# Performance work log

Hardware: AMD Instinct MI355X
Metric: run time of the kernel (lower is better)

Reference implementation:

```python
import jax, jax.numpy as jnp
from jax import lax
import numpy as np

N, F_IN, D_MODEL = 8192, 128, 256
D_INNER, D_STATE, D_CONV, DT_RANK = 512, 16, 4, 16  # expand=2, d_state=16, d_conv=4, dt_rank=ceil(256/16)
BN_EPS = 1e-5


def setup_inputs() -> dict:
    key = jax.random.key(0)
    ks = jax.random.split(key, 12)
    rn = lambda k, s, sc: jax.random.normal(k, s, jnp.float32) * sc
    x = rn(ks[0], (N, F_IN), 1.0)
    # normalized dense adjacency (row sums ~1)
    adj = jax.random.uniform(ks[1], (N, N), jnp.float32) * (2.0 / N)
    w_gcn = rn(ks[2], (F_IN, D_MODEL), 1.0 / np.sqrt(F_IN))
    b_gcn = rn(ks[3], (D_MODEL,), 0.02)
    bn_gamma = jnp.ones((D_MODEL,), jnp.float32)
    bn_beta = jnp.zeros((D_MODEL,), jnp.float32)
    w_in = rn(ks[4], (2 * D_INNER, D_MODEL), 1.0 / np.sqrt(D_MODEL))
    conv_w = rn(ks[5], (D_INNER, D_CONV), 1.0 / np.sqrt(D_CONV))
    conv_b = rn(ks[6], (D_INNER,), 0.02)
    w_xproj = rn(ks[7], (DT_RANK + 2 * D_STATE, D_INNER), 1.0 / np.sqrt(D_INNER))
    w_dt = rn(ks[8], (D_INNER, DT_RANK), 1.0 / np.sqrt(DT_RANK))
    b_dt = rn(ks[9], (D_INNER,), 0.1)
    A_log = jnp.log(jnp.broadcast_to(jnp.arange(1, D_STATE + 1, dtype=jnp.float32), (D_INNER, D_STATE)))
    D_skip = jnp.ones((D_INNER,), jnp.float32)
    w_out = rn(ks[10], (D_MODEL, D_INNER), 1.0 / np.sqrt(D_INNER))
    return dict(x=x, adj=adj, w_gcn=w_gcn, b_gcn=b_gcn, bn_gamma=bn_gamma, bn_beta=bn_beta,
                w_in=w_in, conv_w=conv_w, conv_b=conv_b, w_xproj=w_xproj, w_dt=w_dt,
                b_dt=b_dt, A_log=A_log, D_skip=D_skip, w_out=w_out)


def _forward(x, adj, w_gcn, b_gcn, bn_gamma, bn_beta, w_in, conv_w, conv_b,
             w_xproj, w_dt, b_dt, A_log, D_skip, w_out):
    # --- GCN layer: adj @ (x @ W) + b ---
    h = adj @ (x @ w_gcn) + b_gcn            # (N, D_MODEL)
    h = jax.nn.relu(h)
    # dropout: eval mode -> identity
    # --- BatchNorm1d (batch statistics, biased var, as torch training norm) ---
    mean = jnp.mean(h, axis=0)
    var = jnp.var(h, axis=0)
    h = (h - mean) * lax.rsqrt(var + BN_EPS) * bn_gamma + bn_beta  # (N, D_MODEL)

    # --- Mamba block, batch=1, seq_len=N ---
    xz = h @ w_in.T                          # (N, 2*D_INNER)
    xm, z = jnp.split(xz, 2, axis=-1)        # (N, D_INNER) each

    # causal depthwise conv1d (kernel D_CONV) + SiLU
    xp = jnp.pad(xm, ((D_CONV - 1, 0), (0, 0)))
    xc = conv_b + sum(xp[i:i + N] * conv_w[:, i] for i in range(D_CONV))  # (N, D_INNER)
    xc = jax.nn.silu(xc)

    # input-dependent SSM parameters
    x_dbl = xc @ w_xproj.T                   # (N, DT_RANK + 2*D_STATE)
    dt_r = x_dbl[:, :DT_RANK]
    B = x_dbl[:, DT_RANK:DT_RANK + D_STATE]  # (N, D_STATE)
    C = x_dbl[:, DT_RANK + D_STATE:]         # (N, D_STATE)
    dt = jax.nn.softplus(dt_r @ w_dt.T + b_dt)  # (N, D_INNER)

    A = -jnp.exp(A_log)                      # (D_INNER, D_STATE)
    deltaA = jnp.exp(dt[:, :, None] * A[None])                 # (N, D_INNER, D_STATE)
    deltaBu = dt[:, :, None] * B[:, None, :] * xc[:, :, None]  # (N, D_INNER, D_STATE)

    def step(hs, inp):
        dA, dBu, c = inp
        hs = dA * hs + dBu                   # (D_INNER, D_STATE)
        return hs, hs @ c                    # emit (D_INNER,)

    h0 = jnp.zeros((D_INNER, D_STATE), xc.dtype)
    _, ys = lax.scan(step, h0, (deltaA, deltaBu, C))  # ys: (N, D_INNER)

    y = ys + D_skip * xc
    y = y * jax.nn.silu(z)
    out_m = y @ w_out.T                      # (N, D_MODEL)
    return out_m + h                         # residual


def reference(x, adj, w_gcn, b_gcn, bn_gamma, bn_beta, w_in, conv_w, conv_b,
              w_xproj, w_dt, b_dt, A_log, D_skip, w_out):
    return _forward(x, adj, w_gcn, b_gcn, bn_gamma, bn_beta, w_in, conv_w, conv_b,
                    w_xproj, w_dt, b_dt, A_log, D_skip, w_out)
```

## Files before the change

kernel.cpp:

```cpp
#include <hip/hip_runtime.h>
#include <hip/hip_bf16.h>
#include <stdint.h>

#define NN   8192
#define FIN  128
#define DM   256
#define DI   512
#define DST  16
#define NC   128
#define CL   64

typedef short bf16x8 __attribute__((ext_vector_type(8)));
typedef float f32x4 __attribute__((ext_vector_type(4)));

union FragU { unsigned u[4]; uint4 u4; bf16x8 v; };

__device__ __forceinline__ unsigned short f2bf(float x){
  unsigned u = __float_as_uint(x);
  return (unsigned short)((u + 0x7FFFu + ((u >> 16) & 1u)) >> 16);
}
__device__ __forceinline__ unsigned pack2(float a, float b){
  return (unsigned)f2bf(a) | ((unsigned)f2bf(b) << 16);
}
__device__ __forceinline__ float sigmoidf_(float x){ return 1.f / (1.f + __expf(-x)); }
__device__ __forceinline__ f32x4 zero4(){ f32x4 z; z[0]=0.f; z[1]=0.f; z[2]=0.f; z[3]=0.f; return z; }

constexpr size_t OFF_XWT   = 0;
constexpr size_t OFF_H     = OFF_XWT   + (size_t)DM*NN*2;
constexpr size_t OFF_HBN   = OFF_H     + (size_t)NN*DM*4;
constexpr size_t OFF_HBNB  = OFF_HBN   + (size_t)NN*DM*4;
constexpr size_t OFF_WINB  = OFF_HBNB  + (size_t)NN*DM*2;
constexpr size_t OFF_WXPB  = OFF_WINB  + (size_t)1024*256*2;
constexpr size_t OFF_WOUTB = OFF_WXPB  + (size_t)48*512*2;
constexpr size_t OFF_XZ    = OFF_WOUTB + (size_t)256*512*2;
constexpr size_t OFF_XC    = OFF_XZ    + (size_t)NN*1024*4;
constexpr size_t OFF_XCB   = OFF_XC    + (size_t)NN*DI*4;
constexpr size_t OFF_XDBL  = OFF_XCB   + (size_t)NN*DI*2;
constexpr size_t OFF_DT    = OFF_XDBL  + (size_t)NN*48*4;
constexpr size_t OFF_P     = OFF_DT    + (size_t)NN*DI*4;
constexpr size_t OFF_F     = OFF_P     + (size_t)NC*DI*DST*4;
constexpr size_t OFF_CARRY = OFF_F     + (size_t)NC*DI*DST*4;
constexpr size_t OFF_YB    = OFF_CARRY + (size_t)NC*DI*DST*4;
constexpr size_t OFF_BNS   = OFF_YB    + (size_t)NN*DI*2;
constexpr size_t OFF_BNS2  = OFF_BNS   + 256*4;
constexpr size_t WS_NEED   = OFF_BNS2  + 256*4;

__global__ __launch_bounds__(256) void prep_kernel(
    const float* __restrict__ w_in, const float* __restrict__ w_xp, const float* __restrict__ w_out,
    unsigned short* __restrict__ o_in, unsigned short* __restrict__ o_xp, unsigned short* __restrict__ o_out)
{
  int i = blockIdx.x * 256 + threadIdx.x;
  if (i < 1024*256) o_in[i]  = f2bf(w_in[i]);
  if (i < 48*512)   o_xp[i]  = f2bf(w_xp[i]);
  if (i < 256*512)  o_out[i] = f2bf(w_out[i]);
}

__global__ __launch_bounds__(256) void gemm1_kernel(
    const float* __restrict__ x, const float* __restrict__ w, unsigned short* __restrict__ xwT)
{
  __shared__ float xs[16*128];
  const int t = threadIdx.x;
  const int m0 = blockIdx.x * 16;
  {
    int r = t >> 4, c0 = (t & 15) * 8;
    const float* src = x + (size_t)(m0 + r)*FIN + c0;
    *(float4*)&xs[r*128 + c0]     = *(const float4*)src;
    *(float4*)&xs[r*128 + c0 + 4] = *(const float4*)(src + 4);
  }
  __syncthreads();
  const int n = t;
  float acc[16];
  #pragma unroll
  for (int m = 0; m < 16; ++m) acc[m] = 0.f;
  for (int k = 0; k < 128; k += 4){
    float w0 = w[(size_t)k*DM + n];
    float w1 = w[(size_t)(k+1)*DM + n];
    float w2 = w[(size_t)(k+2)*DM + n];
    float w3 = w[(size_t)(k+3)*DM + n];
    #pragma unroll
    for (int m = 0; m < 16; ++m){
      float4 xv = *(const float4*)&xs[m*128 + k];
      acc[m] = fmaf(xv.x, w0, acc[m]);
      acc[m] = fmaf(xv.y, w1, acc[m]);
      acc[m] = fmaf(xv.z, w2, acc[m]);
      acc[m] = fmaf(xv.w, w3, acc[m]);
    }
  }
  unsigned outp[8];
  #pragma unroll
  for (int m = 0; m < 8; ++m) outp[m] = pack2(acc[2*m], acc[2*m+1]);
  unsigned short* dst = xwT + (size_t)n*NN + m0;
  ((uint4*)dst)[0] = *(uint4*)&outp[0];
  ((uint4*)dst)[1] = *(uint4*)&outp[4];
}

__global__ __launch_bounds__(512) void gemm2_kernel(
    const float* __restrict__ adj, const unsigned short* __restrict__ xwT,
    const float* __restrict__ b_gcn, float* __restrict__ h,
    float* __restrict__ bn_sum, float* __restrict__ bn_sumsq)
{
  __shared__ unsigned a_lds[32*34];
  const int t = threadIdx.x;
  const int wave = t >> 6, lane = t & 63, r = lane & 15, q = lane >> 4;
  const int m0 = blockIdx.x * 32;
  const int nw = wave * 32;

  f32x4 acc[2][2];
  #pragma unroll
  for (int mi = 0; mi < 2; ++mi)
    #pragma unroll
    for (int ni = 0; ni < 2; ++ni) acc[mi][ni] = zero4();

  const int srow = t >> 4;
  const int scol = (t & 15) * 4;
  const float* aptr = adj + (size_t)(m0 + srow)*NN + scol;
  const unsigned short* bp0 = xwT + (size_t)(nw + r)*NN;
  const unsigned short* bp1 = xwT + (size_t)(nw + 16 + r)*NN;

  float4 av = *(const float4*)aptr;

  for (int k0 = 0; k0 < NN; k0 += 64){
    unsigned u0 = pack2(av.x, av.y);
    unsigned u1 = pack2(av.z, av.w);
    __syncthreads();
    a_lds[srow*34 + (t&15)*2]     = u0;
    a_lds[srow*34 + (t&15)*2 + 1] = u1;
    __syncthreads();
    if (k0 + 64 < NN) av = *(const float4*)(aptr + k0 + 64);
    #pragma unroll
    for (int kk = 0; kk < 64; kk += 32){
      FragU fa[2], fb[2];
      #pragma unroll
      for (int mi = 0; mi < 2; ++mi){
        int w0 = (mi*16 + r)*34 + (kk >> 1) + q*4;
        uint2 p0 = *(const uint2*)&a_lds[w0];
        uint2 p1 = *(const uint2*)&a_lds[w0 + 2];
        fa[mi].u[0] = p0.x; fa[mi].u[1] = p0.y; fa[mi].u[2] = p1.x; fa[mi].u[3] = p1.y;
      }
      fb[0].u4 = *(const uint4*)(bp0 + k0 + kk + q*8);
      fb[1].u4 = *(const uint4*)(bp1 + k0 + kk + q*8);
      #pragma unroll
      for (int mi = 0; mi < 2; ++mi)
        #pragma unroll
        for (int ni = 0; ni < 2; ++ni)
          acc[mi][ni] = __builtin_amdgcn_mfma_f32_16x16x32_bf16(fa[mi].v, fb[ni].v, acc[mi][ni], 0, 0, 0);
    }
  }

  #pragma unroll
  for (int ni = 0; ni < 2; ++ni){
    const int n = nw + ni*16 + r;
    const float bias = b_gcn[n];
    float s1 = 0.f, s2 = 0.f;
    #pragma unroll
    for (int mi = 0; mi < 2; ++mi){
      #pragma unroll
      for (int jr = 0; jr < 4; ++jr){
        const int m = m0 + mi*16 + q*4 + jr;
        float v = acc[mi][ni][jr] + bias;
        v = fmaxf(v, 0.f);
        h[(size_t)m*DM + n] = v;
        s1 += v; s2 += v*v;
      }
    }
    s1 += __shfl_xor(s1, 16); s1 += __shfl_xor(s1, 32);
    s2 += __shfl_xor(s2, 16); s2 += __shfl_xor(s2, 32);
    if (q == 0){
      atomicAdd(bn_sum + n, s1);
      atomicAdd(bn_sumsq + n, s2);
    }
  }
}

__global__ __launch_bounds__(256) void bnapply_kernel(
    const float* __restrict__ h, const float* __restrict__ s1, const float* __restrict__ s2,
    const float* __restrict__ gamma, const float* __restrict__ beta,
    float* __restrict__ hbn, unsigned short* __restrict__ hbnb)
{
  int i = blockIdx.x * 256 + threadIdx.x;
  int c = i & (DM - 1);
  float mean = s1[c] * (1.f / NN);
  float var  = s2[c] * (1.f / NN) - mean * mean;
  float inv  = rsqrtf(var + 1e-5f);
  float v = (h[i] - mean) * inv * gamma[c] + beta[c];
  hbn[i] = v;
  hbnb[i] = f2bf(v);
}

__global__ __launch_bounds__(256) void gemm3_kernel(
    const unsigned short* __restrict__ Ab, const unsigned short* __restrict__ Wb, float* __restrict__ xz)
{
  __shared__ unsigned a_lds[64*34];
  const int t = threadIdx.x;
  const int wave = t >> 6, lane = t & 63, r = lane & 15, q = lane >> 4;
  const int wm = wave & 1, wn = wave >> 1;
  const int mb = (blockIdx.x & 127) * 64;
  const int nb = (blockIdx.x >> 7) * 128;

  f32x4 acc[2][4];
  #pragma unroll
  for (int mi = 0; mi < 2; ++mi)
    #pragma unroll
    for (int ni = 0; ni < 4; ++ni) acc[mi][ni] = zero4();

  const int srow = t >> 2;
  const int skoff = (t & 3) * 16;
  const unsigned short* ap = Ab + (size_t)(mb + srow)*DM + skoff;
  const unsigned short* bp = Wb + (size_t)(nb + wn*64 + r)*DM;

  uint4 av0 = *(const uint4*)ap;
  uint4 av1 = *(const uint4*)(ap + 8);

  for (int k0 = 0; k0 < DM; k0 += 64){
    __syncthreads();
    unsigned* dst = &a_lds[srow*34 + (skoff >> 1)];
    dst[0]=av0.x; dst[1]=av0.y; dst[2]=av0.z; dst[3]=av0.w;
    dst[4]=av1.x; dst[5]=av1.y; dst[6]=av1.z; dst[7]=av1.w;
    __syncthreads();
    if (k0 + 64 < DM){ av0 = *(const uint4*)(ap + k0 + 64); av1 = *(const uint4*)(ap + k0 + 64 + 8); }
    #pragma unroll
    for (int kk = 0; kk < 64; kk += 32){
      FragU fa[2], fb[4];
      #pragma unroll
      for (int mi = 0; mi < 2; ++mi){
        int w0 = (wm*32 + mi*16 + r)*34 + (kk >> 1) + q*4;
        uint2 p0 = *(const uint2*)&a_lds[w0];
        uint2 p1 = *(const uint2*)&a_lds[w0 + 2];
        fa[mi].u[0]=p0.x; fa[mi].u[1]=p0.y; fa[mi].u[2]=p1.x; fa[mi].u[3]=p1.y;
      }
      #pragma unroll
      for (int ni = 0; ni < 4; ++ni)
        fb[ni].u4 = *(const uint4*)(bp + (size_t)ni*16*DM + k0 + kk + q*8);
      #pragma unroll
      for (int mi = 0; mi < 2; ++mi)
        #pragma unroll
        for (int ni = 0; ni < 4; ++ni)
          acc[mi][ni] = __builtin_amdgcn_mfma_f32_16x16x32_bf16(fa[mi].v, fb[ni].v, acc[mi][ni], 0, 0, 0);
    }
  }
  #pragma unroll
  for (int mi = 0; mi < 2; ++mi)
    #pragma unroll
    for (int ni = 0; ni < 4; ++ni)
      #pragma unroll
      for (int jr = 0; jr < 4; ++jr)
        xz[(size_t)(mb + wm*32 + mi*16 + q*4 + jr)*1024 + nb + wn*64 + ni*16 + r] = acc[mi][ni][jr];
}

__global__ __launch_bounds__(256) void conv_kernel(
    const float* __restrict__ xz, const float* __restrict__ conv_w, const float* __restrict__ conv_b,
    float* __restrict__ xc, unsigned short* __restrict__ xcb)
{
  int i = blockIdx.x * 256 + threadIdx.x;
  int d = i & (DI - 1), n = i >> 9;
  float4 w4 = *(const float4*)(conv_w + d*4);
  float s = conv_b[d];
  const float* col = xz + d;
  if (n >= 3){
    s += col[(size_t)(n-3)*1024]*w4.x + col[(size_t)(n-2)*1024]*w4.y
       + col[(size_t)(n-1)*1024]*w4.z + col[(size_t)n*1024]*w4.w;
  } else {
    float wv[4] = {w4.x, w4.y, w4.z, w4.w};
    #pragma unroll
    for (int j = 0; j < 4; ++j){ int nn2 = n - 3 + j; if (nn2 >= 0) s += col[(size_t)nn2*1024]*wv[j]; }
  }
  float v = s * sigmoidf_(s);
  xc[i] = v;
  xcb[i] = f2bf(v);
}

__global__ __launch_bounds__(256) void gemm4_kernel(
    const unsigned short* __restrict__ Ab, const unsigned short* __restrict__ Wb, float* __restrict__ xdbl)
{
  __shared__ unsigned a_lds[64*34];
  const int t = threadIdx.x;
  const int wave = t >> 6, lane = t & 63, r = lane & 15, q = lane >> 4;
  const int mb = blockIdx.x * 64;

  f32x4 acc[3];
  #pragma unroll
  for (int ni = 0; ni < 3; ++ni) acc[ni] = zero4();

  const int srow = t >> 2;
  const int skoff = (t & 3) * 16;
  const unsigned short* ap = Ab + (size_t)(mb + srow)*DI + skoff;
  const unsigned short* bp = Wb + (size_t)r*DI;

  uint4 av0 = *(const uint4*)ap;
  uint4 av1 = *(const uint4*)(ap + 8);

  for (int k0 = 0; k0 < DI; k0 += 64){
    __syncthreads();
    unsigned* dst = &a_lds[srow*34 + (skoff >> 1)];
    dst[0]=av0.x; dst[1]=av0.y; dst[2]=av0.z; dst[3]=av0.w;
    dst[4]=av1.x; dst[5]=av1.y; dst[6]=av1.z; dst[7]=av1.w;
    __syncthreads();
    if (k0 + 64 < DI){ av0 = *(const uint4*)(ap + k0 + 64); av1 = *(const uint4*)(ap + k0 + 64 + 8); }
    #pragma unroll
    for (int kk = 0; kk < 64; kk += 32){
      FragU fa, fb[3];
      {
        int w0 = (wave*16 + r)*34 + (kk >> 1) + q*4;
        uint2 p0 = *(const uint2*)&a_lds[w0];
        uint2 p1 = *(const uint2*)&a_lds[w0 + 2];
        fa.u[0]=p0.x; fa.u[1]=p0.y; fa.u[2]=p1.x; fa.u[3]=p1.y;
      }
      #pragma unroll
      for (int ni = 0; ni < 3; ++ni)
        fb[ni].u4 = *(const uint4*)(bp + (size_t)ni*16*DI + k0 + kk + q*8);
      #pragma unroll
      for (int ni = 0; ni < 3; ++ni)
        acc[ni] = __builtin_amdgcn_mfma_f32_16x16x32_bf16(fa.v, fb[ni].v, acc[ni], 0, 0, 0);
    }
  }
  #pragma unroll
  for (int ni = 0; ni < 3; ++ni)
    #pragma unroll
    for (int jr = 0; jr < 4; ++jr)
      xdbl[(size_t)(mb + wave*16 + q*4 + jr)*48 + ni*16 + r] = acc[ni][jr];
}

__global__ __launch_bounds__(256) void dt_kernel(
    const float* __restrict__ xdbl, const float* __restrict__ w_dt, const float* __restrict__ b_dt,
    float* __restrict__ dt)
{
  __shared__ float xr[16];
  const int n = blockIdx.x >> 1;
  const int d = ((blockIdx.x & 1) << 8) + threadIdx.x;
  if (threadIdx.x < 16) xr[threadIdx.x] = xdbl[(size_t)n*48 + threadIdx.x];
  __syncthreads();
  float a = b_dt[d];
  const float4* wp = (const float4*)(w_dt + d*16);
  const float4* xp = (const float4*)xr;
  #pragma unroll
  for (int j = 0; j < 4; ++j){
    float4 w4 = wp[j]; float4 x4 = xp[j];
    a += w4.x*x4.x + w4.y*x4.y + w4.z*x4.z + w4.w*x4.w;
  }
  float o = (a > 20.f) ? a : log1pf(__expf(a));
  dt[(size_t)n*DI + d] = o;
}

__global__ __launch_bounds__(256) void scanA_kernel(
    const float* __restrict__ dt, const float* __restrict__ xc,
    const float* __restrict__ xdbl, const float* __restrict__ A_log,
    float* __restrict__ Pm, float* __restrict__ Fm)
{
  __shared__ float Bs[CL*DST];
  const int t = threadIdx.x;
  const int c = blockIdx.x >> 1;
  const int d = ((blockIdx.x & 1) << 8) + t;
  #pragma unroll
  for (int j = 0; j < (CL*DST)/256; ++j){
    int idx = t + 256*j;
    Bs[idx] = xdbl[(size_t)(c*CL + (idx >> 4))*48 + 16 + (idx & 15)];
  }
  __syncthreads();
  float Av[DST], hs[DST];
  {
    const float4* Ap = (const float4*)(A_log + d*DST);
    #pragma unroll
    for (int s4 = 0; s4 < 4; ++s4){
      float4 a4 = Ap[s4];
      Av[s4*4+0] = -__expf(a4.x); Av[s4*4+1] = -__expf(a4.y);
      Av[s4*4+2] = -__expf(a4.z); Av[s4*4+3] = -__expf(a4.w);
    }
  }
  #pragma unroll
  for (int s = 0; s < DST; ++s) hs[s] = 0.f;
  float sdt = 0.f;
  for (int tt = 0; tt < CL; ++tt){
    const int tg = c*CL + tt;
    float dtv = dt[(size_t)tg*DI + d];
    float xcv = xc[(size_t)tg*DI + d];
    float u = dtv * xcv;
    sdt += dtv;
    #pragma unroll
    for (int s = 0; s < DST; ++s){
      float dA = __expf(dtv * Av[s]);
      hs[s] = dA*hs[s] + u*Bs[tt*DST + s];
    }
  }
  const size_t base = (size_t)c*(DI*DST) + (size_t)d*DST;
  #pragma unroll
  for (int s = 0; s < DST; ++s) Fm[base + s] = hs[s];
  #pragma unroll
  for (int s = 0; s < DST; ++s) Pm[base + s] = __expf(Av[s]*sdt);
}

__global__ __launch_bounds__(256) void scanB_kernel(
    const float* __restrict__ Pm, const float* __restrict__ Fm, float* __restrict__ Cy)
{
  const int ds = blockIdx.x * 256 + threadIdx.x;
  float cy = 0.f;
  Cy[ds] = 0.f;
  #pragma unroll 4
  for (int c = 1; c < NC; ++c){
    size_t prev = (size_t)(c-1)*(DI*DST) + ds;
    cy = Pm[prev]*cy + Fm[prev];
    Cy[(size_t)c*(DI*DST) + ds] = cy;
  }
}

__global__ __launch_bounds__(256) void scanC_kernel(
    const float* __restrict__ dt, const float* __restrict__ xc,
    const float* __restrict__ xdbl, const float* __restrict__ A_log,
    const float* __restrict__ Cy, const float* __restrict__ Dskip,
    const float* __restrict__ xz, unsigned short* __restrict__ yb)
{
  __shared__ float Bs[CL*DST];
  __shared__ float Cs[CL*DST];
  const int t = threadIdx.x;
  const int c = blockIdx.x >> 1;
  const int d = ((blockIdx.x & 1) << 8) + t;
  #pragma unroll
  for (int j = 0; j < (CL*DST)/256; ++j){
    int idx = t + 256*j;
    int tg = c*CL + (idx >> 4);
    Bs[idx] = xdbl[(size_t)tg*48 + 16 + (idx & 15)];
    Cs[idx] = xdbl[(size_t)tg*48 + 32 + (idx & 15)];
  }
  __syncthreads();
  float Av[DST], hs[DST];
  {
    const float4* Ap = (const float4*)(A_log + d*DST);
    #pragma unroll
    for (int s4 = 0; s4 < 4; ++s4){
      float4 a4 = Ap[s4];
      Av[s4*4+0] = -__expf(a4.x); Av[s4*4+1] = -__expf(a4.y);
      Av[s4*4+2] = -__expf(a4.z); Av[s4*4+3] = -__expf(a4.w);
    }
  }
  {
    const float4* hp = (const float4*)(Cy + (size_t)c*(DI*DST) + (size_t)d*DST);
    #pragma unroll
    for (int s4 = 0; s4 < 4; ++s4){
      float4 h4 = hp[s4];
      hs[s4*4+0] = h4.x; hs[s4*4+1] = h4.y; hs[s4*4+2] = h4.z; hs[s4*4+3] = h4.w;
    }
  }
  const float Dv = Dskip[d];
  for (int tt = 0; tt < CL; ++tt){
    const int tg = c*CL + tt;
    float dtv = dt[(size_t)tg*DI + d];
    float xcv = xc[(size_t)tg*DI + d];
    float u = dtv * xcv;
    float y0 = 0.f, y1 = 0.f;
    #pragma unroll
    for (int s = 0; s < DST; s += 2){
      float dA0 = __expf(dtv * Av[s]);
      float dA1 = __expf(dtv * Av[s+1]);
      hs[s]   = dA0*hs[s]   + u*Bs[tt*DST + s];
      hs[s+1] = dA1*hs[s+1] + u*Bs[tt*DST + s+1];
      y0 += hs[s]   * Cs[tt*DST + s];
      y1 += hs[s+1] * Cs[tt*DST + s+1];
    }
    float zv = xz[(size_t)tg*1024 + 512 + d];
    float yf = ((y0 + y1) + Dv*xcv) * (zv * sigmoidf_(zv));
    yb[(size_t)tg*DI + d] = f2bf(yf);
  }
}

__global__ __launch_bounds__(512) void gemm5_kernel(
    const unsigned short* __restrict__ yb, const unsigned short* __restrict__ Wb,
    const float* __restrict__ hbn, float* __restrict__ out)
{
  __shared__ unsigned a_lds[32*34];
  const int t = threadIdx.x;
  const int wave = t >> 6, lane = t & 63, r = lane & 15, q = lane >> 4;
  const int m0 = blockIdx.x * 32;
  const int nw = wave * 32;

  f32x4 acc[2][2];
  #pragma unroll
  for (int mi = 0; mi < 2; ++mi)
    #pragma unroll
    for (int ni = 0; ni < 2; ++ni) acc[mi][ni] = zero4();

  const int srow = t >> 4;
  const int sc = (t & 15) * 4;
  const unsigned short* ap = yb + (size_t)(m0 + srow)*DI + sc;
  const unsigned short* bp0 = Wb + (size_t)(nw + r)*DI;
  const unsigned short* bp1 = Wb + (size_t)(nw + 16 + r)*DI;

  uint2 av = *(const uint2*)ap;

  for (int k0 = 0; k0 < DI; k0 += 64){
    __syncthreads();
    a_lds[srow*34 + (t&15)*2]     = av.x;
    a_lds[srow*34 + (t&15)*2 + 1] = av.y;
    __syncthreads();
    if (k0 + 64 < DI) av = *(const uint2*)(ap + k0 + 64);
    #pragma unroll
    for (int kk = 0; kk < 64; kk += 32){
      FragU fa[2], fb[2];
      #pragma unroll
      for (int mi = 0; mi < 2; ++mi){
        int w0 = (mi*16 + r)*34 + (kk >> 1) + q*4;
        uint2 p0 = *(const uint2*)&a_lds[w0];
        uint2 p1 = *(const uint2*)&a_lds[w0 + 2];
        fa[mi].u[0]=p0.x; fa[mi].u[1]=p0.y; fa[mi].u[2]=p1.x; fa[mi].u[3]=p1.y;
      }
      fb[0].u4 = *(const uint4*)(bp0 + k0 + kk + q*8);
      fb[1].u4 = *(const uint4*)(bp1 + k0 + kk + q*8);
      #pragma unroll
      for (int mi = 0; mi < 2; ++mi)
        #pragma unroll
        for (int ni = 0; ni < 2; ++ni)
          acc[mi][ni] = __builtin_amdgcn_mfma_f32_16x16x32_bf16(fa[mi].v, fb[ni].v, acc[mi][ni], 0, 0, 0);
    }
  }
  #pragma unroll
  for (int mi = 0; mi < 2; ++mi)
    #pragma unroll
    for (int ni = 0; ni < 2; ++ni){
      const int n = nw + ni*16 + r;
      #pragma unroll
      for (int jr = 0; jr < 4; ++jr){
        size_t idx = (size_t)(m0 + mi*16 + q*4 + jr)*DM + n;
        out[idx] = acc[mi][ni][jr] + hbn[idx];
      }
    }
}

extern "C" void kernel_launch(void* const* d_in, const int* in_sizes, int n_in,
                              void* d_out, int out_size, void* d_ws, size_t ws_size,
                              hipStream_t stream)
{
  const float* x      = (const float*)d_in[0];
  const float* adj    = (const float*)d_in[1];
  const float* w_gcn  = (const float*)d_in[2];
  const float* b_gcn  = (const float*)d_in[3];
  const float* gamma  = (const float*)d_in[4];
  const float* beta   = (const float*)d_in[5];
  const float* w_in   = (const float*)d_in[6];
  const float* conv_w = (const float*)d_in[7];
  const float* conv_b = (const float*)d_in[8];
  const float* w_xp   = (const float*)d_in[9];
  const float* w_dt   = (const float*)d_in[10];
  const float* b_dt   = (const float*)d_in[11];
  const float* A_log  = (const float*)d_in[12];
  const float* D_skip = (const float*)d_in[13];
  const float* w_out  = (const float*)d_in[14];
  float* out = (float*)d_out;
  char* ws = (char*)d_ws;
  if (ws_size < WS_NEED) return;

  unsigned short* xwT   = (unsigned short*)(ws + OFF_XWT);
  float*          h     = (float*)(ws + OFF_H);
  float*          hbn   = (float*)(ws + OFF_HBN);
  unsigned short* hbnb  = (unsigned short*)(ws + OFF_HBNB);
  unsigned short* winb  = (unsigned short*)(ws + OFF_WINB);
  unsigned short* wxpb  = (unsigned short*)(ws + OFF_WXPB);
  unsigned short* woutb = (unsigned short*)(ws + OFF_WOUTB);
  float*          xz    = (float*)(ws + OFF_XZ);
  float*          xc    = (float*)(ws + OFF_XC);
  unsigned short* xcb   = (unsigned short*)(ws + OFF_XCB);
  float*          xdbl  = (float*)(ws + OFF_XDBL);
  float*          dt    = (float*)(ws + OFF_DT);
  float*          Pm    = (float*)(ws + OFF_P);
  float*          Fm    = (float*)(ws + OFF_F);
  float*          Cy    = (float*)(ws + OFF_CARRY);
  unsigned short* yb    = (unsigned short*)(ws + OFF_YB);
  float*          bns   = (float*)(ws + OFF_BNS);
  float*          bns2  = (float*)(ws + OFF_BNS2);

  hipMemsetAsync(bns, 0, 2*256*sizeof(float), stream);

  prep_kernel   <<<1024,  256, 0, stream>>>(w_in, w_xp, w_out, winb, wxpb, woutb);
  gemm1_kernel  <<<512,   256, 0, stream>>>(x, w_gcn, xwT);
  gemm2_kernel  <<<256,   512, 0, stream>>>(adj, xwT, b_gcn, h, bns, bns2);
  bnapply_kernel<<<8192,  256, 0, stream>>>(h, bns, bns2, gamma, beta, hbn, hbnb);
  gemm3_kernel  <<<1024,  256, 0, stream>>>(hbnb, winb, xz);
  conv_kernel   <<<16384, 256, 0, stream>>>(xz, conv_w, conv_b, xc, xcb);
  gemm4_kernel  <<<128,   256, 0, stream>>>(xcb, wxpb, xdbl);
  dt_kernel     <<<16384, 256, 0, stream>>>(xdbl, w_dt, b_dt, dt);
  scanA_kernel  <<<256,   256, 0, stream>>>(dt, xc, xdbl, A_log, Pm, Fm);
  scanB_kernel  <<<32,    256, 0, stream>>>(Pm, Fm, Cy);
  scanC_kernel  <<<256,   256, 0, stream>>>(dt, xc, xdbl, A_log, Cy, D_skip, xz, yb);
  gemm5_kernel  <<<256,   512, 0, stream>>>(yb, woutb, hbn, out);
}
```

Before: 746.7 us.

## Rework pipeline with async LDS loads, split-K adjacency GEMM, bf16 intermediates

The adjacency GEMM now uses 64-row tiles, split-K over two halves, and double-buffered global_load_lds async copies with XOR-swizzled LDS. A separate reduction kernel adds bias, applies ReLU and accumulates BN statistics. Intermediates (h, xm, z, hbn) are stored in bf16 to cut memory traffic. The conv, gemm3/4/5, dt and scan kernels are restructured, with scan chunks halved to 32 steps and more chunks. This changes many stages at once and adds bf16 rounding to the residual and gating inputs.

```diff
diff --git a/kernel.cpp b/kernel.cpp
--- a/kernel.cpp
+++ b/kernel.cpp
@@ -1,5 +1,4 @@
 #include <hip/hip_runtime.h>
-#include <hip/hip_bf16.h>
 #include <stdint.h>
 
 #define NN   8192
@@ -7,12 +6,11 @@
 #define DM   256
 #define DI   512
 #define DST  16
-#define NC   128
-#define CL   64
+#define NC   256
+#define CL   32
 
 typedef short bf16x8 __attribute__((ext_vector_type(8)));
 typedef float f32x4 __attribute__((ext_vector_type(4)));
-
 union FragU { unsigned u[4]; uint4 u4; bf16x8 v; };
 
 __device__ __forceinline__ unsigned short f2bf(float x){
@@ -22,25 +20,41 @@
 __device__ __forceinline__ unsigned pack2(float a, float b){
   return (unsigned)f2bf(a) | ((unsigned)f2bf(b) << 16);
 }
+__device__ __forceinline__ unsigned pack2rn(float a, float b){
+  unsigned ua = __float_as_uint(a) + 0x8000u;
+  unsigned ub = __float_as_uint(b) + 0x8000u;
+  return __builtin_amdgcn_perm(ub, ua, 0x07060302u);
+}
+__device__ __forceinline__ float bf2f(unsigned short u){
+  return __uint_as_float(((unsigned)u) << 16);
+}
 __device__ __forceinline__ float sigmoidf_(float x){ return 1.f / (1.f + __expf(-x)); }
 __device__ __forceinline__ f32x4 zero4(){ f32x4 z; z[0]=0.f; z[1]=0.f; z[2]=0.f; z[3]=0.f; return z; }
 
+#define ASYNC16(g, l) __builtin_amdgcn_global_load_lds( \
+    (const __attribute__((address_space(1))) void*)(g), \
+    (__attribute__((address_space(3))) void*)(l), 16, 0, 0)
+#define WAITVM3  asm volatile("s_waitcnt vmcnt(3)" ::: "memory")
+#define WAITVM0  asm volatile("s_waitcnt vmcnt(0)" ::: "memory")
+#define WAITLGKM0 asm volatile("s_waitcnt lgkmcnt(0)" ::: "memory")
+#define BARRIER  asm volatile("s_barrier" ::: "memory")
+
 constexpr size_t OFF_XWT   = 0;
-constexpr size_t OFF_H     = OFF_XWT   + (size_t)DM*NN*2;
-constexpr size_t OFF_HBN   = OFF_H     + (size_t)NN*DM*4;
-constexpr size_t OFF_HBNB  = OFF_HBN   + (size_t)NN*DM*4;
+constexpr size_t OFF_HP    = OFF_XWT   + (size_t)DM*NN*2;
+constexpr size_t OFF_HB    = OFF_HP    + (size_t)2*NN*DM*4;
+constexpr size_t OFF_HBNB  = OFF_HB    + (size_t)NN*DM*2;
 constexpr size_t OFF_WINB  = OFF_HBNB  + (size_t)NN*DM*2;
 constexpr size_t OFF_WXPB  = OFF_WINB  + (size_t)1024*256*2;
 constexpr size_t OFF_WOUTB = OFF_WXPB  + (size_t)48*512*2;
-constexpr size_t OFF_XZ    = OFF_WOUTB + (size_t)256*512*2;
-constexpr size_t OFF_XC    = OFF_XZ    + (size_t)NN*1024*4;
+constexpr size_t OFF_XMB   = OFF_WOUTB + (size_t)256*512*2;
+constexpr size_t OFF_ZB    = OFF_XMB   + (size_t)NN*DI*2;
+constexpr size_t OFF_XC    = OFF_ZB    + (size_t)NN*DI*2;
 constexpr size_t OFF_XCB   = OFF_XC    + (size_t)NN*DI*4;
 constexpr size_t OFF_XDBL  = OFF_XCB   + (size_t)NN*DI*2;
 constexpr size_t OFF_DT    = OFF_XDBL  + (size_t)NN*48*4;
-constexpr size_t OFF_P     = OFF_DT    + (size_t)NN*DI*4;
-constexpr size_t OFF_F     = OFF_P     + (size_t)NC*DI*DST*4;
-constexpr size_t OFF_CARRY = OFF_F     + (size_t)NC*DI*DST*4;
-constexpr size_t OFF_YB    = OFF_CARRY + (size_t)NC*DI*DST*4;
+constexpr size_t OFF_PF    = OFF_DT    + (size_t)NN*DI*4;
+constexpr size_t OFF_CY    = OFF_PF    + (size_t)NC*DI*DST*8;
+constexpr size_t OFF_YB    = OFF_CY    + (size_t)NC*DI*DST*4;
 constexpr size_t OFF_BNS   = OFF_YB    + (size_t)NN*DI*2;
 constexpr size_t OFF_BNS2  = OFF_BNS   + 256*4;
 constexpr size_t WS_NEED   = OFF_BNS2  + 256*4;
@@ -96,269 +110,385 @@
 
 __global__ __launch_bounds__(512) void gemm2_kernel(
     const float* __restrict__ adj, const unsigned short* __restrict__ xwT,
-    const float* __restrict__ b_gcn, float* __restrict__ h,
-    float* __restrict__ bn_sum, float* __restrict__ bn_sumsq)
-{
-  __shared__ unsigned a_lds[32*34];
+    float* __restrict__ hp)
+{
+  __shared__ char lds[2][24576];
   const int t = threadIdx.x;
   const int wave = t >> 6, lane = t & 63, r = lane & 15, q = lane >> 4;
+  const int mt = (int)blockIdx.x & 127, ks = (int)blockIdx.x >> 7;
+  const int m0 = mt * 64;
+  const int kb = ks * 4096;
+  const int wm = wave & 1, wn = wave >> 1;
+
+  const int arow = t >> 3;
+  const int asg  = (t & 7) ^ (arow & 7);
+  const float* asrc = adj + (size_t)(m0 + arow)*NN + kb + asg*4;
+  const int adst = t * 16;
+  const int bn0 = t >> 2;
+  const int bs0 = (t & 3) ^ ((bn0 >> 1) & 3);
+  const int bn1 = (512 + t) >> 2;
+  const int bs1 = ((512 + t) & 3) ^ ((bn1 >> 1) & 3);
+  const unsigned short* bsrc0 = xwT + (size_t)bn0*NN + kb + bs0*8;
+  const unsigned short* bsrc1 = xwT + (size_t)bn1*NN + kb + bs1*8;
+  const int bdst0 = 8192 + t*16;
+  const int bdst1 = 8192 + (512 + t)*16;
+
+  f32x4 acc[2][4];
+  #pragma unroll
+  for (int mi = 0; mi < 2; ++mi)
+    #pragma unroll
+    for (int ni = 0; ni < 4; ++ni) acc[mi][ni] = zero4();
+
+  ASYNC16(asrc,       lds[0] + adst);
+  ASYNC16(bsrc0,      lds[0] + bdst0);
+  ASYNC16(bsrc1,      lds[0] + bdst1);
+  ASYNC16(asrc + 32,  lds[1] + adst);
+  ASYNC16(bsrc0 + 32, lds[1] + bdst0);
+  ASYNC16(bsrc1 + 32, lds[1] + bdst1);
+
+  const int ar0 = wm*32 + r;
+  const int ar1 = ar0 + 16;
+  const int aoff00 = ar0*32 + (((2*q)   ^ (ar0 & 7)) << 2);
+  const int aoff01 = ar0*32 + (((2*q+1) ^ (ar0 & 7)) << 2);
+  const int aoff10 = ar1*32 + (((2*q)   ^ (ar1 & 7)) << 2);
+  const int aoff11 = ar1*32 + (((2*q+1) ^ (ar1 & 7)) << 2);
+  int boff[4];
+  #pragma unroll
+  for (int ni = 0; ni < 4; ++ni){
+    int nl = wn*64 + ni*16 + r;
+    boff[ni] = nl*4 + (q ^ ((nl >> 1) & 3));
+  }
+
+  #pragma unroll 2
+  for (int k = 0; k < 128; ++k){
+    if (k < 127) { WAITVM3; } else { WAITVM0; }
+    BARRIER;
+    const float* Af = (const float*)lds[k & 1];
+    const uint4* Bf = (const uint4*)(lds[k & 1] + 8192);
+    float4 p00 = *(const float4*)(Af + aoff00);
+    float4 p01 = *(const float4*)(Af + aoff01);
+    float4 p10 = *(const float4*)(Af + aoff10);
+    float4 p11 = *(const float4*)(Af + aoff11);
+    FragU fb[4];
+    #pragma unroll
+    for (int ni = 0; ni < 4; ++ni) fb[ni].u4 = Bf[boff[ni]];
+    WAITLGKM0;
+    BARRIER;
+    if (k + 2 < 128){
+      int k0 = (k + 2) * 32;
+      char* L = lds[k & 1];
+      ASYNC16(asrc + k0,  L + adst);
+      ASYNC16(bsrc0 + k0, L + bdst0);
+      ASYNC16(bsrc1 + k0, L + bdst1);
+    }
+    FragU fa0, fa1;
+    fa0.u[0] = pack2rn(p00.x, p00.y); fa0.u[1] = pack2rn(p00.z, p00.w);
+    fa0.u[2] = pack2rn(p01.x, p01.y); fa0.u[3] = pack2rn(p01.z, p01.w);
+    fa1.u[0] = pack2rn(p10.x, p10.y); fa1.u[1] = pack2rn(p10.z, p10.w);
+    fa1.u[2] = pack2rn(p11.x, p11.y); fa1.u[3] = pack2rn(p11.z, p11.w);
+    #pragma unroll
+    for (int ni = 0; ni < 4; ++ni){
+      acc[0][ni] = __builtin_amdgcn_mfma_f32_16x16x32_bf16(fa0.v, fb[ni].v, acc[0][ni], 0, 0, 0);
+      acc[1][ni] = __builtin_amdgcn_mfma_f32_16x16x32_bf16(fa1.v, fb[ni].v, acc[1][ni], 0, 0, 0);
+    }
+  }
+
+  float* hpo = hp + (size_t)ks * ((size_t)NN * DM);
+  #pragma unroll
+  for (int mi = 0; mi < 2; ++mi)
+    #pragma unroll
+    for (int ni = 0; ni < 4; ++ni){
+      const int n = wn*64 + ni*16 + r;
+      #pragma unroll
+      for (int jr = 0; jr < 4; ++jr){
+        const int m = m0 + wm*32 + mi*16 + q*4 + jr;
+        hpo[(size_t)m*DM + n] = acc[mi][ni][jr];
+      }
+    }
+}
+
+__global__ __launch_bounds__(256) void hred_kernel(
+    const float* __restrict__ hp, const float* __restrict__ b_gcn,
+    unsigned short* __restrict__ hb, float* __restrict__ bns, float* __restrict__ bns2)
+{
+  const int c = threadIdx.x;
   const int m0 = blockIdx.x * 32;
-  const int nw = wave * 32;
-
-  f32x4 acc[2][2];
+  const float bias = b_gcn[c];
+  float s1 = 0.f, s2 = 0.f;
+  #pragma unroll 8
+  for (int rr = 0; rr < 32; ++rr){
+    size_t idx = (size_t)(m0 + rr)*DM + c;
+    float v = hp[idx] + hp[(size_t)NN*DM + idx] + bias;
+    v = fmaxf(v, 0.f);
+    hb[idx] = f2bf(v);
+    s1 += v; s2 += v*v;
+  }
+  atomicAdd(bns + c, s1);
+  atomicAdd(bns2 + c, s2);
+}
+
+__global__ __launch_bounds__(256) void bnapply_kernel(
+    const unsigned short* __restrict__ hb, const float* __restrict__ s1, const float* __restrict__ s2,
+    const float* __restrict__ gamma, const float* __restrict__ beta,
+    unsigned short* __restrict__ hbnb)
+{
+  int base = (blockIdx.x*256 + threadIdx.x) * 2;
+  int c0 = base & (DM - 1);
+  ushort2 hv = *(const ushort2*)(hb + base);
+  float mA = s1[c0] * (1.f/NN),   mB = s1[c0+1] * (1.f/NN);
+  float vA = s2[c0] * (1.f/NN) - mA*mA, vB = s2[c0+1] * (1.f/NN) - mB*mB;
+  float iA = rsqrtf(vA + 1e-5f), iB = rsqrtf(vB + 1e-5f);
+  float a = (bf2f(hv.x) - mA)*iA*gamma[c0]   + beta[c0];
+  float b = (bf2f(hv.y) - mB)*iB*gamma[c0+1] + beta[c0+1];
+  ushort2 o; o.x = f2bf(a); o.y = f2bf(b);
+  *(ushort2*)(hbnb + base) = o;
+}
+
+__global__ __launch_bounds__(256) void gemm3_kernel(
+    const unsigned short* __restrict__ Ab, const unsigned short* __restrict__ Wb,
+    unsigned short* __restrict__ xmb, unsigned short* __restrict__ zb)
+{
+  __shared__ uint4 alds[2048];
+  const int t = threadIdx.x;
+  const int wave = t >> 6, lane = t & 63, r = lane & 15, q = lane >> 4;
+  const int mb = ((int)blockIdx.x & 127) * 64;
+  const int nb = ((int)blockIdx.x >> 7) * 128;
+  const int wm = wave & 1, wn = wave >> 1;
+
+  #pragma unroll
+  for (int j = 0; j < 8; ++j){
+    int si = j*256 + t;
+    int row = si >> 5, dg = si & 31;
+    int sg = dg ^ (row & 31);
+    ASYNC16(Ab + (size_t)(mb + row)*DM + sg*8, (char*)alds + si*16);
+  }
+  __syncthreads();
+
+  f32x4 acc[2][4];
   #pragma unroll
   for (int mi = 0; mi < 2; ++mi)
     #pragma unroll
-    for (int ni = 0; ni < 2; ++ni) acc[mi][ni] = zero4();
-
-  const int srow = t >> 4;
-  const int scol = (t & 15) * 4;
-  const float* aptr = adj + (size_t)(m0 + srow)*NN + scol;
-  const unsigned short* bp0 = xwT + (size_t)(nw + r)*NN;
-  const unsigned short* bp1 = xwT + (size_t)(nw + 16 + r)*NN;
-
-  float4 av = *(const float4*)aptr;
-
-  for (int k0 = 0; k0 < NN; k0 += 64){
-    unsigned u0 = pack2(av.x, av.y);
-    unsigned u1 = pack2(av.z, av.w);
-    __syncthreads();
-    a_lds[srow*34 + (t&15)*2]     = u0;
-    a_lds[srow*34 + (t&15)*2 + 1] = u1;
-    __syncthreads();
-    if (k0 + 64 < NN) av = *(const float4*)(aptr + k0 + 64);
-    #pragma unroll
-    for (int kk = 0; kk < 64; kk += 32){
-      FragU fa[2], fb[2];
-      #pragma unroll
-      for (int mi = 0; mi < 2; ++mi){
-        int w0 = (mi*16 + r)*34 + (kk >> 1) + q*4;
-        uint2 p0 = *(const uint2*)&a_lds[w0];
-        uint2 p1 = *(const uint2*)&a_lds[w0 + 2];
-        fa[mi].u[0] = p0.x; fa[mi].u[1] = p0.y; fa[mi].u[2] = p1.x; fa[mi].u[3] = p1.y;
+    for (int ni = 0; ni < 4; ++ni) acc[mi][ni] = zero4();
+
+  const unsigned short* bp[4];
+  #pragma unroll
+  for (int ni = 0; ni < 4; ++ni)
+    bp[ni] = Wb + (size_t)(nb + wn*64 + ni*16 + r)*DM + q*8;
+  FragU fb[4];
+  #pragma unroll
+  for (int ni = 0; ni < 4; ++ni) fb[ni].u4 = *(const uint4*)bp[ni];
+
+  #pragma unroll
+  for (int it = 0; it < 8; ++it){
+    FragU fbn[4];
+    if (it < 7){
+      #pragma unroll
+      for (int ni = 0; ni < 4; ++ni) fbn[ni].u4 = *(const uint4*)(bp[ni] + (it+1)*32);
+    }
+    FragU fa[2];
+    #pragma unroll
+    for (int mi = 0; mi < 2; ++mi){
+      int row = wm*32 + mi*16 + r;
+      int g = it*4 + q;
+      fa[mi].u4 = alds[row*32 + (g ^ (row & 31))];
+    }
+    #pragma unroll
+    for (int mi = 0; mi < 2; ++mi)
+      #pragma unroll
+      for (int ni = 0; ni < 4; ++ni)
+        acc[mi][ni] = __builtin_amdgcn_mfma_f32_16x16x32_bf16(fa[mi].v, fb[ni].v, acc[mi][ni], 0, 0, 0);
+    if (it < 7){
+      #pragma unroll
+      for (int ni = 0; ni < 4; ++ni) fb[ni] = fbn[ni];
+    }
+  }
+  #pragma unroll
+  for (int mi = 0; mi < 2; ++mi)
+    #pragma unroll
+    for (int ni = 0; ni < 4; ++ni){
+      int nc = nb + wn*64 + ni*16 + r;
+      unsigned short* dst = (nc < 512) ? (xmb + nc) : (zb + (nc - 512));
+      #pragma unroll
+      for (int jr = 0; jr < 4; ++jr){
+        int m = mb + wm*32 + mi*16 + q*4 + jr;
+        dst[(size_t)m*DI] = f2bf(acc[mi][ni][jr]);
       }
-      fb[0].u4 = *(const uint4*)(bp0 + k0 + kk + q*8);
-      fb[1].u4 = *(const uint4*)(bp1 + k0 + kk + q*8);
+    }
+}
+
+__global__ __launch_bounds__(256) void conv_kernel(
+    const unsigned short* __restrict__ xmb, const float* __restrict__ conv_w, const float* __restrict__ conv_b,
+    float* __restrict__ xc, unsigned short* __restrict__ xcb)
+{
+  const int d0 = threadIdx.x * 2;
+  const int n0 = blockIdx.x * 32;
+  float4 wa = *(const float4*)(conv_w + (size_t)d0*4);
+  float4 wb = *(const float4*)(conv_w + (size_t)d0*4 + 4);
+  float2 bias = *(const float2*)(conv_b + d0);
+  float x0a=0.f,x1a=0.f,x2a=0.f, x0b=0.f,x1b=0.f,x2b=0.f;
+  #pragma unroll
+  for (int j = 0; j < 3; ++j){
+    int n = n0 - 3 + j;
+    float va = 0.f, vb = 0.f;
+    if (n >= 0){
+      ushort2 u = *(const ushort2*)(xmb + (size_t)n*DI + d0);
+      va = bf2f(u.x); vb = bf2f(u.y);
+    }
+    if (j == 0){ x0a = va; x0b = vb; }
+    else if (j == 1){ x1a = va; x1b = vb; }
+    else { x2a = va; x2b = vb; }
+  }
+  for (int j = 0; j < 32; ++j){
+    int n = n0 + j;
+    ushort2 u = *(const ushort2*)(xmb + (size_t)n*DI + d0);
+    float x3a = bf2f(u.x), x3b = bf2f(u.y);
+    float sa = bias.x + wa.x*x0a + wa.y*x1a + wa.z*x2a + wa.w*x3a;
+    float sb = bias.y + wb.x*x0b + wb.y*x1b + wb.z*x2b + wb.w*x3b;
+    float va = sa * sigmoidf_(sa);
+    float vb = sb * sigmoidf_(sb);
+    *(float2*)(xc + (size_t)n*DI + d0) = make_float2(va, vb);
+    ushort2 o; o.x = f2bf(va); o.y = f2bf(vb);
+    *(ushort2*)(xcb + (size_t)n*DI + d0) = o;
+    x0a=x1a; x1a=x2a; x2a=x3a;
+    x0b=x1b; x1b=x2b; x2b=x3b;
+  }
+}
+
+__global__ __launch_bounds__(256) void gemm4_kernel(
+    const unsigned short* __restrict__ Ab, const unsigned short* __restrict__ Wb, float* __restrict__ xdbl)
+{
+  __shared__ uint4 alds[2048];
+  const int t = threadIdx.x;
+  const int wave = t >> 6, lane = t & 63, r = lane & 15, q = lane >> 4;
+  const int m0 = (int)blockIdx.x * 32;
+  #pragma unroll
+  for (int j = 0; j < 8; ++j){
+    int si = j*256 + t;
+    int row = si >> 6, dg = si & 63;
+    int sg = dg ^ (row & 31);
+    ASYNC16(Ab + (size_t)(m0 + row)*DI + sg*8, (char*)alds + si*16);
+  }
+  __syncthreads();
+  f32x4 acc[2][3];
+  #pragma unroll
+  for (int mi = 0; mi < 2; ++mi)
+    #pragma unroll
+    for (int ni = 0; ni < 3; ++ni) acc[mi][ni] = zero4();
+  const int kq = wave * 128;
+  const unsigned short* bp[3];
+  #pragma unroll
+  for (int ni = 0; ni < 3; ++ni) bp[ni] = Wb + (size_t)(ni*16 + r)*DI + kq + q*8;
+  FragU fb[3];
+  #pragma unroll
+  for (int ni = 0; ni < 3; ++ni) fb[ni].u4 = *(const uint4*)bp[ni];
+  #pragma unroll
+  for (int it = 0; it < 4; ++it){
+    FragU fbn[3];
+    if (it < 3){
+      #pragma unroll
+      for (int ni = 0; ni < 3; ++ni) fbn[ni].u4 = *(const uint4*)(bp[ni] + (it+1)*32);
+    }
+    FragU fa[2];
+    #pragma unroll
+    for (int mi = 0; mi < 2; ++mi){
+      int row = mi*16 + r;
+      int g = (kq >> 3) + it*4 + q;
+      fa[mi].u4 = alds[row*64 + (g ^ (row & 31))];
+    }
+    #pragma unroll
+    for (int mi = 0; mi < 2; ++mi)
+      #pragma unroll
+      for (int ni = 0; ni < 3; ++ni)
+        acc[mi][ni] = __builtin_amdgcn_mfma_f32_16x16x32_bf16(fa[mi].v, fb[ni].v, acc[mi][ni], 0, 0, 0);
+    if (it < 3){
+      #pragma unroll
+      for (int ni = 0; ni < 3; ++ni) fb[ni] = fbn[ni];
+    }
+  }
+  __syncthreads();
+  float* red = (float*)alds;
+  if (wave > 0){
+    int base = ((wave - 1)*64 + lane)*24;
+    #pragma unroll
+    for (int mi = 0; mi < 2; ++mi)
+      #pragma unroll
+      for (int ni = 0; ni < 3; ++ni)
+        #pragma unroll
+        for (int jr = 0; jr < 4; ++jr)
+          red[base + (mi*3 + ni)*4 + jr] = acc[mi][ni][jr];
+  }
+  __syncthreads();
+  if (wave == 0){
+    #pragma unroll
+    for (int w = 0; w < 3; ++w){
+      int base = (w*64 + lane)*24;
       #pragma unroll
       for (int mi = 0; mi < 2; ++mi)
         #pragma unroll
-        for (int ni = 0; ni < 2; ++ni)
-          acc[mi][ni] = __builtin_amdgcn_mfma_f32_16x16x32_bf16(fa[mi].v, fb[ni].v, acc[mi][ni], 0, 0, 0);
-    }
-  }
-
-  #pragma unroll
-  for (int ni = 0; ni < 2; ++ni){
-    const int n = nw + ni*16 + r;
-    const float bias = b_gcn[n];
-    float s1 = 0.f, s2 = 0.f;
-    #pragma unroll
-    for (int mi = 0; mi < 2; ++mi){
-      #pragma unroll
-      for (int jr = 0; jr < 4; ++jr){
-        const int m = m0 + mi*16 + q*4 + jr;
-        float v = acc[mi][ni][jr] + bias;
-        v = fmaxf(v, 0.f);
-        h[(size_t)m*DM + n] = v;
-        s1 += v; s2 += v*v;
-      }
-    }
-    s1 += __shfl_xor(s1, 16); s1 += __shfl_xor(s1, 32);
-    s2 += __shfl_xor(s2, 16); s2 += __shfl_xor(s2, 32);
-    if (q == 0){
-      atomicAdd(bn_sum + n, s1);
-      atomicAdd(bn_sumsq + n, s2);
-    }
-  }
-}
-
-__global__ __launch_bounds__(256) void bnapply_kernel(
-    const float* __restrict__ h, const float* __restrict__ s1, const float* __restrict__ s2,
-    const float* __restrict__ gamma, const float* __restrict__ beta,
-    float* __restrict__ hbn, unsigned short* __restrict__ hbnb)
-{
-  int i = blockIdx.x * 256 + threadIdx.x;
-  int c = i & (DM - 1);
-  float mean = s1[c] * (1.f / NN);
-  float var  = s2[c] * (1.f / NN) - mean * mean;
-  float inv  = rsqrtf(var + 1e-5f);
-  float v = (h[i] - mean) * inv * gamma[c] + beta[c];
-  hbn[i] = v;
-  hbnb[i] = f2bf(v);
-}
-
-__global__ __launch_bounds__(256) void gemm3_kernel(
-    const unsigned short* __restrict__ Ab, const unsigned short* __restrict__ Wb, float* __restrict__ xz)
-{
-  __shared__ unsigned a_lds[64*34];
-  const int t = threadIdx.x;
-  const int wave = t >> 6, lane = t & 63, r = lane & 15, q = lane >> 4;
-  const int wm = wave & 1, wn = wave >> 1;
-  const int mb = (blockIdx.x & 127) * 64;
-  const int nb = (blockIdx.x >> 7) * 128;
-
-  f32x4 acc[2][4];
-  #pragma unroll
-  for (int mi = 0; mi < 2; ++mi)
-    #pragma unroll
-    for (int ni = 0; ni < 4; ++ni) acc[mi][ni] = zero4();
-
-  const int srow = t >> 2;
-  const int skoff = (t & 3) * 16;
-  const unsigned short* ap = Ab + (size_t)(mb + srow)*DM + skoff;
-  const unsigned short* bp = Wb + (size_t)(nb + wn*64 + r)*DM;
-
-  uint4 av0 = *(const uint4*)ap;
-  uint4 av1 = *(const uint4*)(ap + 8);
-
-  for (int k0 = 0; k0 < DM; k0 += 64){
-    __syncthreads();
-    unsigned* dst = &a_lds[srow*34 + (skoff >> 1)];
-    dst[0]=av0.x; dst[1]=av0.y; dst[2]=av0.z; dst[3]=av0.w;
-    dst[4]=av1.x; dst[5]=av1.y; dst[6]=av1.z; dst[7]=av1.w;
-    __syncthreads();
-    if (k0 + 64 < DM){ av0 = *(const uint4*)(ap + k0 + 64); av1 = *(const uint4*)(ap + k0 + 64 + 8); }
-    #pragma unroll
-    for (int kk = 0; kk < 64; kk += 32){
-      FragU fa[2], fb[4];
-      #pragma unroll
-      for (int mi = 0; mi < 2; ++mi){
-        int w0 = (wm*32 + mi*16 + r)*34 + (kk >> 1) + q*4;
-        uint2 p0 = *(const uint2*)&a_lds[w0];
-        uint2 p1 = *(const uint2*)&a_lds[w0 + 2];
-        fa[mi].u[0]=p0.x; fa[mi].u[1]=p0.y; fa[mi].u[2]=p1.x; fa[mi].u[3]=p1.y;
-      }
-      #pragma unroll
-      for (int ni = 0; ni < 4; ++ni)
-        fb[ni].u4 = *(const uint4*)(bp + (size_t)ni*16*DM + k0 + kk + q*8);
-      #pragma unroll
-      for (int mi = 0; mi < 2; ++mi)
+        for (int ni = 0; ni < 3; ++ni)
+          #pragma unroll
+          for (int jr = 0; jr < 4; ++jr)
+            acc[mi][ni][jr] += red[base + (mi*3 + ni)*4 + jr];
+    }
+    #pragma unroll
+    for (int mi = 0; mi < 2; ++mi)
+      #pragma unroll
+      for (int ni = 0; ni < 3; ++ni)
         #pragma unroll
-        for (int ni = 0; ni < 4; ++ni)
-          acc[mi][ni] = __builtin_amdgcn_mfma_f32_16x16x32_bf16(fa[mi].v, fb[ni].v, acc[mi][ni], 0, 0, 0);
-    }
-  }
-  #pragma unroll
-  for (int mi = 0; mi < 2; ++mi)
-    #pragma unroll
-    for (int ni = 0; ni < 4; ++ni)
-      #pragma unroll
-      for (int jr = 0; jr < 4; ++jr)
-        xz[(size_t)(mb + wm*32 + mi*16 + q*4 + jr)*1024 + nb + wn*64 + ni*16 + r] = acc[mi][ni][jr];
-}
-
-__global__ __launch_bounds__(256) void conv_kernel(
-    const float* __restrict__ xz, const float* __restrict__ conv_w, const float* __restrict__ conv_b,
-    float* __restrict__ xc, unsigned short* __restrict__ xcb)
-{
-  int i = blockIdx.x * 256 + threadIdx.x;
-  int d = i & (DI - 1), n = i >> 9;
-  float4 w4 = *(const float4*)(conv_w + d*4);
-  float s = conv_b[d];
-  const float* col = xz + d;
-  if (n >= 3){
-    s += col[(size_t)(n-3)*1024]*w4.x + col[(size_t)(n-2)*1024]*w4.y
-       + col[(size_t)(n-1)*1024]*w4.z + col[(size_t)n*1024]*w4.w;
-  } else {
-    float wv[4] = {w4.x, w4.y, w4.z, w4.w};
-    #pragma unroll
-    for (int j = 0; j < 4; ++j){ int nn2 = n - 3 + j; if (nn2 >= 0) s += col[(size_t)nn2*1024]*wv[j]; }
-  }
-  float v = s * sigmoidf_(s);
-  xc[i] = v;
-  xcb[i] = f2bf(v);
-}
-
-__global__ __launch_bounds__(256) void gemm4_kernel(
-    const unsigned short* __restrict__ Ab, const unsigned short* __restrict__ Wb, float* __restrict__ xdbl)
-{
-  __shared__ unsigned a_lds[64*34];
-  const int t = threadIdx.x;
-  const int wave = t >> 6, lane = t & 63, r = lane & 15, q = lane >> 4;
-  const int mb = blockIdx.x * 64;
-
-  f32x4 acc[3];
-  #pragma unroll
-  for (int ni = 0; ni < 3; ++ni) acc[ni] = zero4();
-
-  const int srow = t >> 2;
-  const int skoff = (t & 3) * 16;
-  const unsigned short* ap = Ab + (size_t)(mb + srow)*DI + skoff;
-  const unsigned short* bp = Wb + (size_t)r*DI;
-
-  uint4 av0 = *(const uint4*)ap;
-  uint4 av1 = *(const uint4*)(ap + 8);
-
-  for (int k0 = 0; k0 < DI; k0 += 64){
-    __syncthreads();
-    unsigned* dst = &a_lds[srow*34 + (skoff >> 1)];
-    dst[0]=av0.x; dst[1]=av0.y; dst[2]=av0.z; dst[3]=av0.w;
-    dst[4]=av1.x; dst[5]=av1.y; dst[6]=av1.z; dst[7]=av1.w;
-    __syncthreads();
-    if (k0 + 64 < DI){ av0 = *(const uint4*)(ap + k0 + 64); av1 = *(const uint4*)(ap + k0 + 64 + 8); }
-    #pragma unroll
-    for (int kk = 0; kk < 64; kk += 32){
-      FragU fa, fb[3];
-      {
-        int w0 = (wave*16 + r)*34 + (kk >> 1) + q*4;
-        uint2 p0 = *(const uint2*)&a_lds[w0];
-        uint2 p1 = *(const uint2*)&a_lds[w0 + 2];
-        fa.u[0]=p0.x; fa.u[1]=p0.y; fa.u[2]=p1.x; fa.u[3]=p1.y;
-      }
-      #pragma unroll
-      for (int ni = 0; ni < 3; ++ni)
-        fb[ni].u4 = *(const uint4*)(bp + (size_t)ni*16*DI + k0 + kk + q*8);
-      #pragma unroll
-      for (int ni = 0; ni < 3; ++ni)
-        acc[ni] = __builtin_amdgcn_mfma_f32_16x16x32_bf16(fa.v, fb[ni].v, acc[ni], 0, 0, 0);
-    }
-  }
-  #pragma unroll
-  for (int ni = 0; ni < 3; ++ni)
-    #pragma unroll
-    for (int jr = 0; jr < 4; ++jr)
-      xdbl[(size_t)(mb + wave*16 + q*4 + jr)*48 + ni*16 + r] = acc[ni][jr];
+        for (int jr = 0; jr < 4; ++jr)
+          xdbl[(size_t)(m0 + mi*16 + q*4 + jr)*48 + ni*16 + r] = acc[mi][ni][jr];
+  }
 }
 
 __global__ __launch_bounds__(256) void dt_kernel(
     const float* __restrict__ xdbl, const float* __restrict__ w_dt, const float* __restrict__ b_dt,
     float* __restrict__ dt)
 {
-  __shared__ float xr[16];
-  const int n = blockIdx.x >> 1;
-  const int d = ((blockIdx.x & 1) << 8) + threadIdx.x;
-  if (threadIdx.x < 16) xr[threadIdx.x] = xdbl[(size_t)n*48 + threadIdx.x];
-  __syncthreads();
-  float a = b_dt[d];
-  const float4* wp = (const float4*)(w_dt + d*16);
-  const float4* xp = (const float4*)xr;
+  __shared__ float xr[64*16];
+  const int t = threadIdx.x;
+  const int dg = (int)blockIdx.x & 1;
+  const int n0 = ((int)blockIdx.x >> 1) * 64;
+  const int d = dg*256 + t;
   #pragma unroll
   for (int j = 0; j < 4; ++j){
-    float4 w4 = wp[j]; float4 x4 = xp[j];
-    a += w4.x*x4.x + w4.y*x4.y + w4.z*x4.z + w4.w*x4.w;
-  }
-  float o = (a > 20.f) ? a : log1pf(__expf(a));
-  dt[(size_t)n*DI + d] = o;
+    int idx = t + 256*j;
+    xr[idx] = xdbl[(size_t)(n0 + (idx >> 4))*48 + (idx & 15)];
+  }
+  __syncthreads();
+  const float4* wp = (const float4*)(w_dt + (size_t)d*16);
+  float4 w0 = wp[0], w1 = wp[1], w2 = wp[2], w3 = wp[3];
+  float bias = b_dt[d];
+  for (int j = 0; j < 64; ++j){
+    const float4* xp = (const float4*)(xr + j*16);
+    float4 a0 = xp[0], a1 = xp[1], a2 = xp[2], a3 = xp[3];
+    float a = bias;
+    a += w0.x*a0.x + w0.y*a0.y + w0.z*a0.z + w0.w*a0.w;
+    a += w1.x*a1.x + w1.y*a1.y + w1.z*a1.z + w1.w*a1.w;
+    a += w2.x*a2.x + w2.y*a2.y + w2.z*a2.z + w2.w*a2.w;
+    a += w3.x*a3.x + w3.y*a3.y + w3.z*a3.z + w3.w*a3.w;
+    float o = (a > 20.f) ? a : log1pf(__expf(a));
+    dt[(size_t)(n0 + j)*DI + d] = o;
+  }
 }
 
 __global__ __launch_bounds__(256) void scanA_kernel(
     const float* __restrict__ dt, const float* __restrict__ xc,
     const float* __restrict__ xdbl, const float* __restrict__ A_log,
-    float* __restrict__ Pm, float* __restrict__ Fm)
+    float2* __restrict__ PF)
 {
   __shared__ float Bs[CL*DST];
   const int t = threadIdx.x;
-  const int c = blockIdx.x >> 1;
-  const int d = ((blockIdx.x & 1) << 8) + t;
-  #pragma unroll
-  for (int j = 0; j < (CL*DST)/256; ++j){
+  const int c = (int)blockIdx.x >> 1;
+  const int d = (((int)blockIdx.x & 1) << 8) + t;
+  #pragma unroll
+  for (int j = 0; j < 2; ++j){
     int idx = t + 256*j;
     Bs[idx] = xdbl[(size_t)(c*CL + (idx >> 4))*48 + 16 + (idx & 15)];
   }
   __syncthreads();
   float Av[DST], hs[DST];
   {
-    const float4* Ap = (const float4*)(A_log + d*DST);
+    const float4* Ap = (const float4*)(A_log + (size_t)d*DST);
     #pragma unroll
     for (int s4 = 0; s4 < 4; ++s4){
       float4 a4 = Ap[s4];
@@ -369,36 +499,66 @@
   #pragma unroll
   for (int s = 0; s < DST; ++s) hs[s] = 0.f;
   float sdt = 0.f;
+  const size_t rb = (size_t)c*CL*DI + d;
+  float dtv = dt[rb], xcv = xc[rb];
   for (int tt = 0; tt < CL; ++tt){
-    const int tg = c*CL + tt;
-    float dtv = dt[(size_t)tg*DI + d];
-    float xcv = xc[(size_t)tg*DI + d];
+    float dtn = 0.f, xcn = 0.f;
+    if (tt + 1 < CL){
+      dtn = dt[rb + (size_t)(tt+1)*DI];
+      xcn = xc[rb + (size_t)(tt+1)*DI];
+    }
     float u = dtv * xcv;
     sdt += dtv;
-    #pragma unroll
-    for (int s = 0; s < DST; ++s){
-      float dA = __expf(dtv * Av[s]);
-      hs[s] = dA*hs[s] + u*Bs[tt*DST + s];
-    }
-  }
-  const size_t base = (size_t)c*(DI*DST) + (size_t)d*DST;
-  #pragma unroll
-  for (int s = 0; s < DST; ++s) Fm[base + s] = hs[s];
-  #pragma unroll
-  for (int s = 0; s < DST; ++s) Pm[base + s] = __expf(Av[s]*sdt);
-}
-
-__global__ __launch_bounds__(256) void scanB_kernel(
-    const float* __restrict__ Pm, const float* __restrict__ Fm, float* __restrict__ Cy)
-{
-  const int ds = blockIdx.x * 256 + threadIdx.x;
+    float bv[DST];
+    *(float4*)&bv[0]  = *(const float4*)&Bs[tt*16];
+    *(float4*)&bv[4]  = *(const float4*)&Bs[tt*16 + 4];
+    *(float4*)&bv[8]  = *(const float4*)&Bs[tt*16 + 8];
+    *(float4*)&bv[12] = *(const float4*)&Bs[tt*16 + 12];
+    #pragma unroll
+    for (int s = 0; s < DST; ++s)
+      hs[s] = __expf(dtv * Av[s]) * hs[s] + u * bv[s];
+    dtv = dtn; xcv = xcn;
+  }
+  float4* out = (float4*)(PF + (size_t)c*(DI*DST) + (size_t)d*DST);
+  #pragma unroll
+  for (int j = 0; j < 8; ++j){
+    float4 v;
+    v.x = __expf(Av[2*j] * sdt);   v.y = hs[2*j];
+    v.z = __expf(Av[2*j+1] * sdt); v.w = hs[2*j+1];
+    out[j] = v;
+  }
+}
+
+__global__ __launch_bounds__(128) void scanB_kernel(
+    const float2* __restrict__ PF, float* __restrict__ Cy)
+{
+  const int ds = (int)blockIdx.x*128 + (int)threadIdx.x;
+  float2 A0[16], A1[16];
+  #pragma unroll
+  for (int j = 0; j < 16; ++j) A0[j] = PF[(size_t)j*8192 + ds];
+  #pragma unroll
+  for (int j = 0; j < 16; ++j) A1[j] = PF[(size_t)(16 + j)*8192 + ds];
   float cy = 0.f;
   Cy[ds] = 0.f;
-  #pragma unroll 4
-  for (int c = 1; c < NC; ++c){
-    size_t prev = (size_t)(c-1)*(DI*DST) + ds;
-    cy = Pm[prev]*cy + Fm[prev];
-    Cy[(size_t)c*(DI*DST) + ds] = cy;
+  #pragma unroll
+  for (int g = 0; g < 16; ++g){
+    #pragma unroll
+    for (int j = 0; j < 16; ++j){
+      int i = g*16 + j;
+      if (i < NC - 1){
+        float2 pf = (g & 1) ? A1[j] : A0[j];
+        cy = pf.x * cy + pf.y;
+        Cy[(size_t)(i + 1)*8192 + ds] = cy;
+      }
+    }
+    int gn = g + 2;
+    if (gn < 16){
+      #pragma unroll
+      for (int j = 0; j < 16; ++j){
+        float2 v = PF[(size_t)(gn*16 + j)*8192 + ds];
+        if (g & 1) A1[j] = v; else A0[j] = v;
+      }
+    }
   }
 }
 
@@ -406,15 +566,15 @@
     const float* __restrict__ dt, const float* __restrict__ xc,
     const float* __restrict__ xdbl, const float* __restrict__ A_log,
     const float* __restrict__ Cy, const float* __restrict__ Dskip,
-    const float* __restrict__ xz, unsigned short* __restrict__ yb)
+    const unsigned short* __restrict__ zb, unsigned short* __restrict__ yb)
 {
   __shared__ float Bs[CL*DST];
   __shared__ float Cs[CL*DST];
   const int t = threadIdx.x;
-  const int c = blockIdx.x >> 1;
-  const int d = ((blockIdx.x & 1) << 8) + t;
-  #pragma unroll
-  for (int j = 0; j < (CL*DST)/256; ++j){
+  const int c = (int)blockIdx.x >> 1;
+  const int d = (((int)blockIdx.x & 1) << 8) + t;
+  #pragma unroll
+  for (int j = 0; j < 2; ++j){
     int idx = t + 256*j;
     int tg = c*CL + (idx >> 4);
     Bs[idx] = xdbl[(size_t)tg*48 + 16 + (idx & 15)];
@@ -423,7 +583,7 @@
   __syncthreads();
   float Av[DST], hs[DST];
   {
-    const float4* Ap = (const float4*)(A_log + d*DST);
+    const float4* Ap = (const float4*)(A_log + (size_t)d*DST);
     #pragma unroll
     for (int s4 = 0; s4 < 4; ++s4){
       float4 a4 = Ap[s4];
@@ -432,83 +592,96 @@
     }
   }
   {
-    const float4* hp = (const float4*)(Cy + (size_t)c*(DI*DST) + (size_t)d*DST);
+    const float4* hp4 = (const float4*)(Cy + (size_t)c*(DI*DST) + (size_t)d*DST);
     #pragma unroll
     for (int s4 = 0; s4 < 4; ++s4){
-      float4 h4 = hp[s4];
+      float4 h4 = hp4[s4];
       hs[s4*4+0] = h4.x; hs[s4*4+1] = h4.y; hs[s4*4+2] = h4.z; hs[s4*4+3] = h4.w;
     }
   }
   const float Dv = Dskip[d];
+  const size_t rb = (size_t)c*CL*DI + d;
+  float dtv = dt[rb], xcv = xc[rb];
+  unsigned short zv0 = zb[rb];
   for (int tt = 0; tt < CL; ++tt){
-    const int tg = c*CL + tt;
-    float dtv = dt[(size_t)tg*DI + d];
-    float xcv = xc[(size_t)tg*DI + d];
+    float dtn = 0.f, xcn = 0.f;
+    unsigned short zn = 0;
+    if (tt + 1 < CL){
+      dtn = dt[rb + (size_t)(tt+1)*DI];
+      xcn = xc[rb + (size_t)(tt+1)*DI];
+      zn  = zb[rb + (size_t)(tt+1)*DI];
+    }
     float u = dtv * xcv;
+    float bv[DST], cv[DST];
+    *(float4*)&bv[0]  = *(const float4*)&Bs[tt*16];
+    *(float4*)&bv[4]  = *(const float4*)&Bs[tt*16 + 4];
+    *(float4*)&bv[8]  = *(const float4*)&Bs[tt*16 + 8];
+    *(float4*)&bv[12] = *(const float4*)&Bs[tt*16 + 12];
+    *(float4*)&cv[0]  = *(const float4*)&Cs[tt*16];
+    *(float4*)&cv[4]  = *(const float4*)&Cs[tt*16 + 4];
+    *(float4*)&cv[8]  = *(const float4*)&Cs[tt*16 + 8];
+    *(float4*)&cv[12] = *(const float4*)&Cs[tt*16 + 12];
     float y0 = 0.f, y1 = 0.f;
     #pragma unroll
     for (int s = 0; s < DST; s += 2){
-      float dA0 = __expf(dtv * Av[s]);
-      float dA1 = __expf(dtv * Av[s+1]);
-      hs[s]   = dA0*hs[s]   + u*Bs[tt*DST + s];
-      hs[s+1] = dA1*hs[s+1] + u*Bs[tt*DST + s+1];
-      y0 += hs[s]   * Cs[tt*DST + s];
-      y1 += hs[s+1] * Cs[tt*DST + s+1];
-    }
-    float zv = xz[(size_t)tg*1024 + 512 + d];
-    float yf = ((y0 + y1) + Dv*xcv) * (zv * sigmoidf_(zv));
-    yb[(size_t)tg*DI + d] = f2bf(yf);
+      hs[s]   = __expf(dtv * Av[s])   * hs[s]   + u * bv[s];
+      hs[s+1] = __expf(dtv * Av[s+1]) * hs[s+1] + u * bv[s+1];
+      y0 += hs[s]   * cv[s];
+      y1 += hs[s+1] * cv[s+1];
+    }
+    float z = bf2f(zv0);
+    float yf = ((y0 + y1) + Dv * xcv) * (z * sigmoidf_(z));
+    yb[rb + (size_t)tt*DI] = f2bf(yf);
+    dtv = dtn; xcv = xcn; zv0 = zn;
   }
 }
 
 __global__ __launch_bounds__(512) void gemm5_kernel(
     const unsigned short* __restrict__ yb, const unsigned short* __restrict__ Wb,
-    const float* __restrict__ hbn, float* __restrict__ out)
-{
-  __shared__ unsigned a_lds[32*34];
+    const unsigned short* __restrict__ hbnb, float* __restrict__ out)
+{
+  __shared__ uint4 alds[2048];
   const int t = threadIdx.x;
   const int wave = t >> 6, lane = t & 63, r = lane & 15, q = lane >> 4;
-  const int m0 = blockIdx.x * 32;
+  const int m0 = (int)blockIdx.x * 32;
+  #pragma unroll
+  for (int j = 0; j < 4; ++j){
+    int si = j*512 + t;
+    int row = si >> 6, dg = si & 63;
+    int sg = dg ^ (row & 31);
+    ASYNC16(yb + (size_t)(m0 + row)*DI + sg*8, (char*)alds + si*16);
+  }
+  __syncthreads();
+  f32x4 acc[2][2];
+  #pragma unroll
+  for (int mi = 0; mi < 2; ++mi)
+    #pragma unroll
+    for (int ni = 0; ni < 2; ++ni) acc[mi][ni] = zero4();
   const int nw = wave * 32;
-
-  f32x4 acc[2][2];
-  #pragma unroll
-  for (int mi = 0; mi < 2; ++mi)
-    #pragma unroll
-    for (int ni = 0; ni < 2; ++ni) acc[mi][ni] = zero4();
-
-  const int srow = t >> 4;
-  const int sc = (t & 15) * 4;
-  const unsigned short* ap = yb + (size_t)(m0 + srow)*DI + sc;
-  const unsigned short* bp0 = Wb + (size_t)(nw + r)*DI;
-  const unsigned short* bp1 = Wb + (size_t)(nw + 16 + r)*DI;
-
-  uint2 av = *(const uint2*)ap;
-
-  for (int k0 = 0; k0 < DI; k0 += 64){
-    __syncthreads();
-    a_lds[srow*34 + (t&15)*2]     = av.x;
-    a_lds[srow*34 + (t&15)*2 + 1] = av.y;
-    __syncthreads();
-    if (k0 + 64 < DI) av = *(const uint2*)(ap + k0 + 64);
-    #pragma unroll
-    for (int kk = 0; kk < 64; kk += 32){
-      FragU fa[2], fb[2];
-      #pragma unroll
-      for (int mi = 0; mi < 2; ++mi){
-        int w0 = (mi*16 + r)*34 + (kk >> 1) + q*4;
-        uint2 p0 = *(const uint2*)&a_lds[w0];
-        uint2 p1 = *(const uint2*)&a_lds[w0 + 2];
-        fa[mi].u[0]=p0.x; fa[mi].u[1]=p0.y; fa[mi].u[2]=p1.x; fa[mi].u[3]=p1.y;
-      }
-      fb[0].u4 = *(const uint4*)(bp0 + k0 + kk + q*8);
-      fb[1].u4 = *(const uint4*)(bp1 + k0 + kk + q*8);
-      #pragma unroll
-      for (int mi = 0; mi < 2; ++mi)
-        #pragma unroll
-        for (int ni = 0; ni < 2; ++ni)
-          acc[mi][ni] = __builtin_amdgcn_mfma_f32_16x16x32_bf16(fa[mi].v, fb[ni].v, acc[mi][ni], 0, 0, 0);
-    }
+  const unsigned short* bp0 = Wb + (size_t)(nw + r)*DI + q*8;
+  const unsigned short* bp1 = Wb + (size_t)(nw + 16 + r)*DI + q*8;
+  FragU fb0, fb1;
+  fb0.u4 = *(const uint4*)bp0;
+  fb1.u4 = *(const uint4*)bp1;
+  #pragma unroll
+  for (int it = 0; it < 16; ++it){
+    FragU fn0, fn1;
+    if (it < 15){
+      fn0.u4 = *(const uint4*)(bp0 + (it+1)*32);
+      fn1.u4 = *(const uint4*)(bp1 + (it+1)*32);
+    }
+    FragU fa[2];
+    #pragma unroll
+    for (int mi = 0; mi < 2; ++mi){
+      int row = mi*16 + r;
+      int g = it*4 + q;
+      fa[mi].u4 = alds[row*64 + (g ^ (row & 31))];
+    }
+    acc[0][0] = __builtin_amdgcn_mfma_f32_16x16x32_bf16(fa[0].v, fb0.v, acc[0][0], 0, 0, 0);
+    acc[0][1] = __builtin_amdgcn_mfma_f32_16x16x32_bf16(fa[0].v, fb1.v, acc[0][1], 0, 0, 0);
+    acc[1][0] = __builtin_amdgcn_mfma_f32_16x16x32_bf16(fa[1].v, fb0.v, acc[1][0], 0, 0, 0);
+    acc[1][1] = __builtin_amdgcn_mfma_f32_16x16x32_bf16(fa[1].v, fb1.v, acc[1][1], 0, 0, 0);
+    if (it < 15){ fb0 = fn0; fb1 = fn1; }
   }
   #pragma unroll
   for (int mi = 0; mi < 2; ++mi)
@@ -517,8 +690,9 @@
       const int n = nw + ni*16 + r;
       #pragma unroll
       for (int jr = 0; jr < 4; ++jr){
-        size_t idx = (size_t)(m0 + mi*16 + q*4 + jr)*DM + n;
-        out[idx] = acc[mi][ni][jr] + hbn[idx];
+        const int m = m0 + mi*16 + q*4 + jr;
+        size_t idx = (size_t)m*DM + n;
+        out[idx] = acc[mi][ni][jr] + bf2f(hbnb[idx]);
       }
     }
 }
@@ -547,36 +721,37 @@
   if (ws_size < WS_NEED) return;
 
   unsigned short* xwT   = (unsigned short*)(ws + OFF_XWT);
-  float*          h     = (float*)(ws + OFF_H);
-  float*          hbn   = (float*)(ws + OFF_HBN);
+  float*          hp    = (float*)(ws + OFF_HP);
+  unsigned short* hb    = (unsigned short*)(ws + OFF_HB);
   unsigned short* hbnb  = (unsigned short*)(ws + OFF_HBNB);
   unsigned short* winb  = (unsigned short*)(ws + OFF_WINB);
   unsigned short* wxpb  = (unsigned short*)(ws + OFF_WXPB);
   unsigned short* woutb = (unsigned short*)(ws + OFF_WOUTB);
-  float*          xz    = (float*)(ws + OFF_XZ);
+  unsigned short* xmb   = (unsigned short*)(ws + OFF_XMB);
+  unsigned short* zb    = (unsigned short*)(ws + OFF_ZB);
   float*          xc    = (float*)(ws + OFF_XC);
   unsigned short* xcb   = (unsigned short*)(ws + OFF_XCB);
   float*          xdbl  = (float*)(ws + OFF_XDBL);
-  float*          dt    = (float*)(ws + OFF_DT);
-  float*          Pm    = (float*)(ws + OFF_P);
-  float*          Fm    = (float*)(ws + OFF_F);
-  float*          Cy    = (float*)(ws + OFF_CARRY);
+  float*          dtb   = (float*)(ws + OFF_DT);
+  float2*         PF    = (float2*)(ws + OFF_PF);
+  float*          Cy    = (float*)(ws + OFF_CY);
   unsigned short* yb    = (unsigned short*)(ws + OFF_YB);
   float*          bns   = (float*)(ws + OFF_BNS);
   float*          bns2  = (float*)(ws + OFF_BNS2);
 
   hipMemsetAsync(bns, 0, 2*256*sizeof(float), stream);
 
-  prep_kernel   <<<1024,  256, 0, stream>>>(w_in, w_xp, w_out, winb, wxpb, woutb);
-  gemm1_kernel  <<<512,   256, 0, stream>>>(x, w_gcn, xwT);
-  gemm2_kernel  <<<256,   512, 0, stream>>>(adj, xwT, b_gcn, h, bns, bns2);
-  bnapply_kernel<<<8192,  256, 0, stream>>>(h, bns, bns2, gamma, beta, hbn, hbnb);
-  gemm3_kernel  <<<1024,  256, 0, stream>>>(hbnb, winb, xz);
-  conv_kernel   <<<16384, 256, 0, stream>>>(xz, conv_w, conv_b, xc, xcb);
-  gemm4_kernel  <<<128,   256, 0, stream>>>(xcb, wxpb, xdbl);
-  dt_kernel     <<<16384, 256, 0, stream>>>(xdbl, w_dt, b_dt, dt);
-  scanA_kernel  <<<256,   256, 0, stream>>>(dt, xc, xdbl, A_log, Pm, Fm);
-  scanB_kernel  <<<32,    256, 0, stream>>>(Pm, Fm, Cy);
-  scanC_kernel  <<<256,   256, 0, stream>>>(dt, xc, xdbl, A_log, Cy, D_skip, xz, yb);
-  gemm5_kernel  <<<256,   512, 0, stream>>>(yb, woutb, hbn, out);
-}
+  prep_kernel   <<<1024, 256, 0, stream>>>(w_in, w_xp, w_out, winb, wxpb, woutb);
+  gemm1_kernel  <<<512,  256, 0, stream>>>(x, w_gcn, xwT);
+  gemm2_kernel  <<<256,  512, 0, stream>>>(adj, xwT, hp);
+  hred_kernel   <<<256,  256, 0, stream>>>(hp, b_gcn, hb, bns, bns2);
+  bnapply_kernel<<<4096, 256, 0, stream>>>(hb, bns, bns2, gamma, beta, hbnb);
+  gemm3_kernel  <<<1024, 256, 0, stream>>>(hbnb, winb, xmb, zb);
+  conv_kernel   <<<256,  256, 0, stream>>>(xmb, conv_w, conv_b, xc, xcb);
+  gemm4_kernel  <<<256,  256, 0, stream>>>(xcb, wxpb, xdbl);
+  dt_kernel     <<<256,  256, 0, stream>>>(xdbl, w_dt, b_dt, dtb);
+  scanA_kernel  <<<512,  256, 0, stream>>>(dtb, xc, xdbl, A_log, PF);
+  scanB_kernel  <<<64,   128, 0, stream>>>(PF, Cy);
+  scanC_kernel  <<<512,  256, 0, stream>>>(dtb, xc, xdbl, A_log, Cy, D_skip, zb, yb);
+  gemm5_kernel  <<<256,  512, 0, stream>>>(yb, woutb, hbnb, out);
+}
```

Result: faster. 629.8 us (-15.7%).
